# Performance work log

Hardware: AMD Instinct MI355X
Metric: run time of the kernel (lower is better)

## Reference

```python
import jax, jax.numpy as jnp
import numpy as np

NUM_HEADS = 12

def setup_inputs() -> dict:
    key = jax.random.key(0)
    k1, k2, k3, k4 = jax.random.split(key, 4)
    B, N, D = 8, 1024, 768
    x = jax.random.normal(k1, (B, N, D), dtype=jnp.float32)
    mask = jax.random.randint(k2, (B, N), 0, 2, dtype=jnp.int32)
    Wqkv = jax.random.normal(k3, (3 * D, D), dtype=jnp.float32) * (D ** -0.5)
    Wproj = jax.random.normal(k4, (D, D), dtype=jnp.float32) * (D ** -0.5)
    bproj = jnp.zeros((D,), dtype=jnp.float32)
    return {"x": x, "mask": mask, "Wqkv": Wqkv, "Wproj": Wproj, "bproj": bproj}

def reference(x, mask, Wqkv, Wproj, bproj):
    B, N, D = x.shape
    H = NUM_HEADS
    hd = D // H
    scale = hd ** -0.5
    # QKV projection (no bias), split into q,k,v of shape [B,H,N,hd]
    qkv = jnp.einsum('bnd,ed->bne', x, Wqkv).reshape(B, N, 3, H, hd)
    qkv = jnp.transpose(qkv, (2, 0, 3, 1, 4))
    q, k, v = qkv[0], qkv[1], qkv[2]
    # padding mask: attend where both query and key are valid; masked-out
    # (padded) query rows attend only to themselves (diagonal) to avoid NaNs
    m = mask.astype(bool)  # [B,N]
    pair = m[:, None, :, None] & m[:, None, None, :]          # [B,1,N,N]
    diag = jnp.eye(N, dtype=bool)[None, None]                 # [1,1,N,N]
    attn_mask = pair | (diag & ~m[:, None, :, None])          # [B,1,N,N]
    scores = jnp.einsum('bhnd,bhmd->bhnm', q, k) * scale      # [B,H,N,N]
    scores = jnp.where(attn_mask, scores, jnp.finfo(scores.dtype).min)
    attn = jax.nn.softmax(scores, axis=-1)
    out = jnp.einsum('bhnm,bhmd->bhnd', attn, v)
    out = jnp.transpose(out, (0, 2, 1, 3)).reshape(B, N, D)
    out = jnp.einsum('bnd,ed->bne', out, Wproj) + bproj
    return out
```

## Files before the change

kernel.cpp:

```cpp
#include <hip/hip_runtime.h>
#include <hip/hip_bf16.h>
#include <stdint.h>


typedef unsigned short u16;
typedef __attribute__((ext_vector_type(8))) short short8;
typedef __attribute__((ext_vector_type(4))) float f32x4;

#define MFMA16(a, b, c) __builtin_amdgcn_mfma_f32_16x16x32_bf16((a), (b), (c), 0, 0, 0)

static __device__ __forceinline__ float bf2f(u16 u) {
    return __uint_as_float(((unsigned int)u) << 16);
}
static __device__ __forceinline__ u16 f2bf(float f) {
    __hip_bfloat16 h = __float2bfloat16(f);
    return *(u16*)&h;
}
static __device__ __forceinline__ void gld16(const u16* g, u16* l) {
  __builtin_amdgcn_global_load_lds(
      (const __attribute__((address_space(1))) void*)g,
      (__attribute__((address_space(3))) void*)l, 16, 0, 0);
}

__global__ __launch_bounds__(256) void cvt_bf16(
    const float* __restrict__ s0, u16* __restrict__ d0, int n0,
    const float* __restrict__ s1, u16* __restrict__ d1, int n1,
    const float* __restrict__ s2, u16* __restrict__ d2, int n2) {
  int i = (blockIdx.x * 256 + threadIdx.x) * 4;
  const float* s; u16* d;
  if (i < n0) { s = s0 + i; d = d0 + i; }
  else if ((i -= n0) < n1) { s = s1 + i; d = d1 + i; }
  else if ((i -= n1) < n2) { s = s2 + i; d = d2 + i; }
  else return;
  float4 v = *(const float4*)s;
  ushort4 o;
  o.x = f2bf(v.x); o.y = f2bf(v.y); o.z = f2bf(v.z); o.w = f2bf(v.w);
  *(ushort4*)d = o;
}

template<int K, int LDC, bool BF16OUT>
__global__ __launch_bounds__(256) void gemm_bt(
    const u16* __restrict__ A,
    const u16* __restrict__ B,
    void* __restrict__ Cout,
    const float* __restrict__ bias) {
  __shared__ u16 As[128 * 32];
  __shared__ u16 Bs[128 * 32];
  const int tid = threadIdx.x;
  const int w = tid >> 6, l = tid & 63;
  const int lane16 = l & 15, quad = l >> 4;
  const int i0 = blockIdx.y * 128, j0 = blockIdx.x * 128;
  const int mh = (w & 1) * 64;
  const int nh = (w >> 1) * 64;

  f32x4 acc[4][4];
  #pragma unroll
  for (int mt = 0; mt < 4; mt++)
    #pragma unroll
    for (int nt = 0; nt < 4; nt++) acc[mt][nt] = (f32x4){0.f, 0.f, 0.f, 0.f};

  for (int kt = 0; kt < K / 32; kt++) {
    const int k0 = kt * 32;
    __syncthreads();
    #pragma unroll
    for (int s = 0; s < 2; s++) {
      int idx = tid + s * 256;
      int row = idx >> 2, c8 = (idx & 3) * 8;
      gld16(&A[(size_t)(i0 + row) * K + k0 + c8], &As[row * 32 + c8]);
      gld16(&B[(size_t)(j0 + row) * K + k0 + c8], &Bs[row * 32 + c8]);
    }
    __syncthreads();

    short8 af[4], bf[4];
    #pragma unroll
    for (int mt = 0; mt < 4; mt++)
      af[mt] = *(const short8*)&As[(mh + mt * 16 + lane16) * 32 + quad * 8];
    #pragma unroll
    for (int nt = 0; nt < 4; nt++)
      bf[nt] = *(const short8*)&Bs[(nh + nt * 16 + lane16) * 32 + quad * 8];
    #pragma unroll
    for (int mt = 0; mt < 4; mt++)
      #pragma unroll
      for (int nt = 0; nt < 4; nt++)
        acc[mt][nt] = MFMA16(af[mt], bf[nt], acc[mt][nt]);
  }

  #pragma unroll
  for (int mt = 0; mt < 4; mt++) {
    #pragma unroll
    for (int nt = 0; nt < 4; nt++) {
      int col = j0 + nh + nt * 16 + lane16;
      #pragma unroll
      for (int r = 0; r < 4; r++) {
        int row = i0 + mh + mt * 16 + quad * 4 + r;
        if (BF16OUT) {
          ((u16*)Cout)[(size_t)row * LDC + col] = f2bf(acc[mt][nt][r]);
        } else {
          ((float*)Cout)[(size_t)row * LDC + col] = acc[mt][nt][r] + bias[col];
        }
      }
    }
  }
}

__global__ __launch_bounds__(256, 3) void attn_mfma(
    const u16* __restrict__ qkv,
    const int* __restrict__ mask,
    u16* __restrict__ ctx) {
  __shared__ u16 Ks[64][72];
  __shared__ u16 Vt[64][72];
  __shared__ u16 Ps[4][32][72];
  __shared__ float mkb[64];
  __shared__ int mqs[128];

  const int tid = threadIdx.x;
  const int w = tid >> 6, l = tid & 63;
  const int lane16 = l & 15, quad = l >> 4;
  const int bh = blockIdx.x >> 3, rb = blockIdx.x & 7;
  const int b = bh / 12, h = bh % 12;
  const int n0 = rb * 128;
  const int baseRow = b * 1024;

  if (tid < 128) mqs[tid] = mask[baseRow + n0 + tid];

  short8 qfrag[2][2];
  #pragma unroll
  for (int mt = 0; mt < 2; mt++) {
    const u16* qp = qkv + (size_t)(baseRow + n0 + w*32 + mt*16 + lane16) * 2304 + h*64;
    #pragma unroll
    for (int ks = 0; ks < 2; ks++)
      qfrag[mt][ks] = *(const short8*)(qp + ks*32 + quad*8);
  }

  f32x4 oacc[2][4];
  #pragma unroll
  for (int mt = 0; mt < 2; mt++)
    #pragma unroll
    for (int nt = 0; nt < 4; nt++) oacc[mt][nt] = (f32x4){0.f, 0.f, 0.f, 0.f};
  float lsum[2][4];
  #pragma unroll
  for (int mt = 0; mt < 2; mt++)
    #pragma unroll
    for (int r = 0; r < 4; r++) lsum[mt][r] = 0.f;

  __syncthreads();
  int mqbits = 0;
  #pragma unroll
  for (int mt = 0; mt < 2; mt++)
    #pragma unroll
    for (int r = 0; r < 4; r++)
      mqbits |= (mqs[w*32 + mt*16 + quad*4 + r] ? 1 : 0) << (mt*4 + r);

  const float K1 = 0.18033688011112043f;
  const float K0 = -23.083120654223415f;

  for (int c = 0; c < 16; c++) {
    __syncthreads();
    {
      int key = tid >> 2, ds = (tid & 3) * 16;
      const u16* kp = qkv + (size_t)(baseRow + c*64 + key) * 2304 + 768 + h*64 + ds;
      *(uint4*)&Ks[key][ds]     = *(const uint4*)kp;
      *(uint4*)&Ks[key][ds + 8] = *(const uint4*)(kp + 8);
      int kA = (tid & 31) * 2, dg = tid >> 5;
      const u16* vp = qkv + (size_t)(baseRow + c*64 + kA) * 2304 + 1536 + h*64 + dg*8;
      uint4 r0 = *(const uint4*)vp;
      uint4 r1 = *(const uint4*)(vp + 2304);
      const u16* va = (const u16*)&r0;
      const u16* vb = (const u16*)&r1;
      #pragma unroll
      for (int j = 0; j < 8; j++)
        *(unsigned int*)&Vt[dg*8 + j][kA] = (unsigned int)va[j] | ((unsigned int)vb[j] << 16);
      if (tid < 64) mkb[tid] = mask[baseRow + c*64 + tid] ? 0.f : -1e38f;
    }
    __syncthreads();

    f32x4 sacc[2][4];
    #pragma unroll
    for (int mt = 0; mt < 2; mt++)
      #pragma unroll
      for (int t = 0; t < 4; t++) sacc[mt][t] = (f32x4){0.f, 0.f, 0.f, 0.f};
    #pragma unroll
    for (int ks = 0; ks < 2; ks++) {
      short8 kf[4];
      #pragma unroll
      for (int t = 0; t < 4; t++)
        kf[t] = *(const short8*)&Ks[t*16 + lane16][ks*32 + quad*8];
      #pragma unroll
      for (int mt = 0; mt < 2; mt++)
        #pragma unroll
        for (int t = 0; t < 4; t++)
          sacc[mt][t] = MFMA16(qfrag[mt][ks], kf[t], sacc[mt][t]);
    }

    #pragma unroll
    for (int t = 0; t < 4; t++) {
      float bias = mkb[t*16 + lane16];
      int cg = c*64 + t*16 + lane16;
      #pragma unroll
      for (int mt = 0; mt < 2; mt++) {
        #pragma unroll
        for (int r = 0; r < 4; r++) {
          float e = __builtin_amdgcn_exp2f(fmaf(sacc[mt][t][r], K1, K0) + bias);
          int rg = n0 + w*32 + mt*16 + quad*4 + r;
          if (!((mqbits >> (mt*4 + r)) & 1)) e = (cg == rg) ? 1.0f : 0.0f;
          lsum[mt][r] += e;
          Ps[w][mt*16 + quad*4 + r][t*16 + lane16] = f2bf(e);
        }
      }
    }

    #pragma unroll
    for (int kc = 0; kc < 2; kc++) {
      short8 pf[2], vf[4];
      #pragma unroll
      for (int mt = 0; mt < 2; mt++)
        pf[mt] = *(const short8*)&Ps[w][mt*16 + lane16][kc*32 + quad*8];
      #pragma unroll
      for (int nt = 0; nt < 4; nt++)
        vf[nt] = *(const short8*)&Vt[nt*16 + lane16][kc*32 + quad*8];
      #pragma unroll
      for (int mt = 0; mt < 2; mt++)
        #pragma unroll
        for (int nt = 0; nt < 4; nt++)
          oacc[mt][nt] = MFMA16(pf[mt], vf[nt], oacc[mt][nt]);
    }
  }

  float linv[2][4];
  #pragma unroll
  for (int mt = 0; mt < 2; mt++)
    #pragma unroll
    for (int r = 0; r < 4; r++) {
      float s = lsum[mt][r];
      s += __shfl_xor(s, 1); s += __shfl_xor(s, 2);
      s += __shfl_xor(s, 4); s += __shfl_xor(s, 8);
      linv[mt][r] = 1.0f / s;
    }
  #pragma unroll
  for (int mt = 0; mt < 2; mt++) {
    #pragma unroll
    for (int nt = 0; nt < 4; nt++) {
      #pragma unroll
      for (int r = 0; r < 4; r++) {
        int rg = n0 + w*32 + mt*16 + quad*4 + r;
        ctx[(size_t)(baseRow + rg) * 768 + h*64 + nt*16 + lane16] =
            f2bf(oacc[mt][nt][r] * linv[mt][r]);
      }
    }
  }
}

extern "C" void kernel_launch(void* const* d_in, const int* in_sizes, int n_in,
                              void* d_out, int out_size, void* d_ws, size_t ws_size,
                              hipStream_t stream) {
  const float* x     = (const float*)d_in[0];
  const int*   mask  = (const int*)d_in[1];
  const float* Wqkv  = (const float*)d_in[2];
  const float* Wproj = (const float*)d_in[3];
  const float* bproj = (const float*)d_in[4];
  float* out = (float*)d_out;

  const int NX = 8192 * 768;
  const int NQ = 2304 * 768;
  const int NP = 768 * 768;

  char* wsb = (char*)d_ws;
  u16* qkv    = (u16*)wsb;
  u16* ctx    = (u16*)(wsb + (size_t)8192 * 2304 * 2);
  u16* xb     = (u16*)(wsb + (size_t)8192 * 2304 * 2 + (size_t)8192 * 768 * 2);
  u16* wqkvb  = xb + NX;
  u16* wprojb = wqkvb + NQ;

  int cvt_blocks = ((NX + NQ + NP) / 4 + 255) / 256;
  cvt_bf16<<<dim3(cvt_blocks), 256, 0, stream>>>(x, xb, NX, Wqkv, wqkvb, NQ, Wproj, wprojb, NP);

  gemm_bt<768, 2304, true><<<dim3(18, 64), 256, 0, stream>>>(xb, wqkvb, qkv, nullptr);
  attn_mfma<<<dim3(768), 256, 0, stream>>>(qkv, mask, ctx);
  gemm_bt<768, 768, false><<<dim3(6, 64), 256, 0, stream>>>(ctx, wprojb, out, bproj);
}
```

Measured before the change: 207.5 us.

## Double-buffer K/V tiles with register prefetch and transpose score MFMA

The attention kernel now double-buffers K, V and the key-mask bias in shared memory and prefetches the tile two chunks ahead into registers. This overlaps global loads with compute and cuts the loop to one barrier per chunk. The score MFMA operands are swapped (K times Q), so each lane holds four consecutive keys for one query and can write P as packed 8-byte stores; the row sum is reduced across quads and redistributed by shuffle. LDS use roughly doubles and launch bounds drop from 3 to 2 blocks per CU, which can lower occupancy.

```diff
diff --git a/kernel.cpp b/kernel.cpp
--- a/kernel.cpp
+++ b/kernel.cpp
@@ -103,14 +103,14 @@
   }
 }
 
-__global__ __launch_bounds__(256, 3) void attn_mfma(
+__global__ __launch_bounds__(256, 2) void attn_mfma(
     const u16* __restrict__ qkv,
     const int* __restrict__ mask,
     u16* __restrict__ ctx) {
-  __shared__ u16 Ks[64][72];
-  __shared__ u16 Vt[64][72];
+  __shared__ u16 Ks[2][64][72];
+  __shared__ u16 Vt[2][64][72];
   __shared__ u16 Ps[4][32][72];
-  __shared__ float mkb[64];
+  __shared__ float mkb[2][64];
   __shared__ int mqs[128];
 
   const int tid = threadIdx.x;
@@ -121,91 +121,107 @@
   const int n0 = rb * 128;
   const int baseRow = b * 1024;
 
+  const int key_s = tid >> 2, ds_s = (tid & 3) * 16;
+  const int kA_s = (tid & 31) * 2, dg_s = tid >> 5;
+
   if (tid < 128) mqs[tid] = mask[baseRow + n0 + tid];
 
   short8 qfrag[2][2];
   #pragma unroll
-  for (int mt = 0; mt < 2; mt++) {
-    const u16* qp = qkv + (size_t)(baseRow + n0 + w*32 + mt*16 + lane16) * 2304 + h*64;
+  for (int qt = 0; qt < 2; qt++) {
+    const u16* qp = qkv + (size_t)(baseRow + n0 + w*32 + qt*16 + lane16) * 2304 + h*64;
     #pragma unroll
     for (int ks = 0; ks < 2; ks++)
-      qfrag[mt][ks] = *(const short8*)(qp + ks*32 + quad*8);
+      qfrag[qt][ks] = *(const short8*)(qp + ks*32 + quad*8);
   }
 
   f32x4 oacc[2][4];
   #pragma unroll
-  for (int mt = 0; mt < 2; mt++)
-    #pragma unroll
-    for (int nt = 0; nt < 4; nt++) oacc[mt][nt] = (f32x4){0.f, 0.f, 0.f, 0.f};
-  float lsum[2][4];
-  #pragma unroll
-  for (int mt = 0; mt < 2; mt++)
-    #pragma unroll
-    for (int r = 0; r < 4; r++) lsum[mt][r] = 0.f;
-
+  for (int qt = 0; qt < 2; qt++)
+    #pragma unroll
+    for (int nt = 0; nt < 4; nt++) oacc[qt][nt] = (f32x4){0.f, 0.f, 0.f, 0.f};
+  float lsum[2] = {0.f, 0.f};
+
+  uint4 kr0[2], kr1[2], vr0[2], vr1[2];
+  int mkv[2];
+
+  auto issue = [&](int c, int rbuf) {
+    const u16* kp = qkv + (size_t)(baseRow + c*64 + key_s) * 2304 + 768 + h*64 + ds_s;
+    kr0[rbuf] = *(const uint4*)kp;
+    kr1[rbuf] = *(const uint4*)(kp + 8);
+    const u16* vp = qkv + (size_t)(baseRow + c*64 + kA_s) * 2304 + 1536 + h*64 + dg_s*8;
+    vr0[rbuf] = *(const uint4*)vp;
+    vr1[rbuf] = *(const uint4*)(vp + 2304);
+    mkv[rbuf] = (tid < 64) ? mask[baseRow + c*64 + tid] : 0;
+  };
+  auto commit = [&](int c, int rbuf) {
+    int lb = c & 1;
+    *(uint4*)&Ks[lb][key_s][ds_s]     = kr0[rbuf];
+    *(uint4*)&Ks[lb][key_s][ds_s + 8] = kr1[rbuf];
+    const u16* va = (const u16*)&vr0[rbuf];
+    const u16* vb = (const u16*)&vr1[rbuf];
+    #pragma unroll
+    for (int j = 0; j < 8; j++)
+      *(unsigned int*)&Vt[lb][dg_s*8 + j][kA_s] =
+          (unsigned int)va[j] | ((unsigned int)vb[j] << 16);
+    if (tid < 64) mkb[lb][tid] = mkv[rbuf] ? 0.f : -1e38f;
+  };
+
+  issue(0, 0); commit(0, 0); issue(1, 1);
   __syncthreads();
-  int mqbits = 0;
-  #pragma unroll
-  for (int mt = 0; mt < 2; mt++)
-    #pragma unroll
-    for (int r = 0; r < 4; r++)
-      mqbits |= (mqs[w*32 + mt*16 + quad*4 + r] ? 1 : 0) << (mt*4 + r);
+
+  int qrg[2]; int mqv[2];
+  #pragma unroll
+  for (int qt = 0; qt < 2; qt++) {
+    qrg[qt] = n0 + w*32 + qt*16 + lane16;
+    mqv[qt] = mqs[w*32 + qt*16 + lane16];
+  }
 
   const float K1 = 0.18033688011112043f;
   const float K0 = -23.083120654223415f;
 
   for (int c = 0; c < 16; c++) {
     __syncthreads();
-    {
-      int key = tid >> 2, ds = (tid & 3) * 16;
-      const u16* kp = qkv + (size_t)(baseRow + c*64 + key) * 2304 + 768 + h*64 + ds;
-      *(uint4*)&Ks[key][ds]     = *(const uint4*)kp;
-      *(uint4*)&Ks[key][ds + 8] = *(const uint4*)(kp + 8);
-      int kA = (tid & 31) * 2, dg = tid >> 5;
-      const u16* vp = qkv + (size_t)(baseRow + c*64 + kA) * 2304 + 1536 + h*64 + dg*8;
-      uint4 r0 = *(const uint4*)vp;
-      uint4 r1 = *(const uint4*)(vp + 2304);
-      const u16* va = (const u16*)&r0;
-      const u16* vb = (const u16*)&r1;
-      #pragma unroll
-      for (int j = 0; j < 8; j++)
-        *(unsigned int*)&Vt[dg*8 + j][kA] = (unsigned int)va[j] | ((unsigned int)vb[j] << 16);
-      if (tid < 64) mkb[tid] = mask[baseRow + c*64 + tid] ? 0.f : -1e38f;
-    }
-    __syncthreads();
-
-    f32x4 sacc[2][4];
-    #pragma unroll
-    for (int mt = 0; mt < 2; mt++)
-      #pragma unroll
-      for (int t = 0; t < 4; t++) sacc[mt][t] = (f32x4){0.f, 0.f, 0.f, 0.f};
-    #pragma unroll
-    for (int ks = 0; ks < 2; ks++) {
-      short8 kf[4];
-      #pragma unroll
-      for (int t = 0; t < 4; t++)
-        kf[t] = *(const short8*)&Ks[t*16 + lane16][ks*32 + quad*8];
-      #pragma unroll
-      for (int mt = 0; mt < 2; mt++)
+    if (c < 15) commit(c + 1, (c + 1) & 1);
+    if (c < 14) issue(c + 2, c & 1);
+    const int lb = c & 1;
+
+    short8 kf[4][2];
+    #pragma unroll
+    for (int kt = 0; kt < 4; kt++)
+      #pragma unroll
+      for (int ks = 0; ks < 2; ks++)
+        kf[kt][ks] = *(const short8*)&Ks[lb][kt*16 + lane16][ks*32 + quad*8];
+    f32x4 sacc[4][2];
+    #pragma unroll
+    for (int kt = 0; kt < 4; kt++)
+      #pragma unroll
+      for (int qt = 0; qt < 2; qt++) sacc[kt][qt] = (f32x4){0.f, 0.f, 0.f, 0.f};
+    #pragma unroll
+    for (int ks = 0; ks < 2; ks++)
+      #pragma unroll
+      for (int kt = 0; kt < 4; kt++)
         #pragma unroll
-        for (int t = 0; t < 4; t++)
-          sacc[mt][t] = MFMA16(qfrag[mt][ks], kf[t], sacc[mt][t]);
-    }
-
-    #pragma unroll
-    for (int t = 0; t < 4; t++) {
-      float bias = mkb[t*16 + lane16];
-      int cg = c*64 + t*16 + lane16;
-      #pragma unroll
-      for (int mt = 0; mt < 2; mt++) {
+        for (int qt = 0; qt < 2; qt++)
+          sacc[kt][qt] = MFMA16(kf[kt][ks], qfrag[qt][ks], sacc[kt][qt]);
+
+    #pragma unroll
+    for (int kt = 0; kt < 4; kt++) {
+      #pragma unroll
+      for (int qt = 0; qt < 2; qt++) {
+        u16 pk[4];
         #pragma unroll
         for (int r = 0; r < 4; r++) {
-          float e = __builtin_amdgcn_exp2f(fmaf(sacc[mt][t][r], K1, K0) + bias);
-          int rg = n0 + w*32 + mt*16 + quad*4 + r;
-          if (!((mqbits >> (mt*4 + r)) & 1)) e = (cg == rg) ? 1.0f : 0.0f;
-          lsum[mt][r] += e;
-          Ps[w][mt*16 + quad*4 + r][t*16 + lane16] = f2bf(e);
+          int keyl = kt*16 + quad*4 + r;
+          float e = __builtin_amdgcn_exp2f(fmaf(sacc[kt][qt][r], K1, K0) + mkb[lb][keyl]);
+          if (!mqv[qt]) e = ((c*64 + keyl) == qrg[qt]) ? 1.0f : 0.0f;
+          lsum[qt] += e;
+          pk[r] = f2bf(e);
         }
+        unsigned int lo = (unsigned int)pk[0] | ((unsigned int)pk[1] << 16);
+        unsigned int hi = (unsigned int)pk[2] | ((unsigned int)pk[3] << 16);
+        uint2 pv; pv.x = lo; pv.y = hi;
+        *(uint2*)&Ps[w][qt*16 + lane16][kt*16 + quad*4] = pv;
       }
     }
 
@@ -213,38 +229,38 @@
     for (int kc = 0; kc < 2; kc++) {
       short8 pf[2], vf[4];
       #pragma unroll
-      for (int mt = 0; mt < 2; mt++)
-        pf[mt] = *(const short8*)&Ps[w][mt*16 + lane16][kc*32 + quad*8];
+      for (int qt = 0; qt < 2; qt++)
+        pf[qt] = *(const short8*)&Ps[w][qt*16 + lane16][kc*32 + quad*8];
       #pragma unroll
       for (int nt = 0; nt < 4; nt++)
-        vf[nt] = *(const short8*)&Vt[nt*16 + lane16][kc*32 + quad*8];
-      #pragma unroll
-      for (int mt = 0; mt < 2; mt++)
+        vf[nt] = *(const short8*)&Vt[lb][nt*16 + lane16][kc*32 + quad*8];
+      #pragma unroll
+      for (int qt = 0; qt < 2; qt++)
         #pragma unroll
         for (int nt = 0; nt < 4; nt++)
-          oacc[mt][nt] = MFMA16(pf[mt], vf[nt], oacc[mt][nt]);
+          oacc[qt][nt] = MFMA16(pf[qt], vf[nt], oacc[qt][nt]);
     }
   }
 
   float linv[2][4];
   #pragma unroll
-  for (int mt = 0; mt < 2; mt++)
-    #pragma unroll
-    for (int r = 0; r < 4; r++) {
-      float s = lsum[mt][r];
-      s += __shfl_xor(s, 1); s += __shfl_xor(s, 2);
-      s += __shfl_xor(s, 4); s += __shfl_xor(s, 8);
-      linv[mt][r] = 1.0f / s;
-    }
-  #pragma unroll
-  for (int mt = 0; mt < 2; mt++) {
+  for (int qt = 0; qt < 2; qt++) {
+    float s = lsum[qt];
+    s += __shfl_xor(s, 16);
+    s += __shfl_xor(s, 32);
+    #pragma unroll
+    for (int r = 0; r < 4; r++)
+      linv[qt][r] = 1.0f / __shfl(s, quad*4 + r);
+  }
+  #pragma unroll
+  for (int qt = 0; qt < 2; qt++) {
     #pragma unroll
     for (int nt = 0; nt < 4; nt++) {
       #pragma unroll
       for (int r = 0; r < 4; r++) {
-        int rg = n0 + w*32 + mt*16 + quad*4 + r;
+        int rg = n0 + w*32 + qt*16 + quad*4 + r;
         ctx[(size_t)(baseRow + rg) * 768 + h*64 + nt*16 + lane16] =
-            f2bf(oacc[mt][nt][r] * linv[mt][r]);
+            f2bf(oacc[qt][nt][r] * linv[qt][r]);
       }
     }
   }
```

Result: slower. 246.4 us (+18.7%).

## Prefetch next K/V tile into registers, hoist masked-row handling to epilogue

Applied to the files above, without the earlier changes.

The attention kernel now issues global loads for the next K/V tile into registers before the current tile's MFMA work and writes them to LDS afterward, so load latency overlaps with compute. Masked query rows no longer get a per-element diagonal select inside the softmax loop. Their output is instead copied directly from the V row in the epilogue, which matches the reference because such a row attends only to itself. The block index mapping is changed so rb varies slowest, and launch bounds are raised to 4 waves per SIMD. The prefetch keeps extra values live in registers, which could conflict with the higher occupancy target.

```diff
diff --git a/kernel.cpp b/kernel.cpp
--- a/kernel.cpp
+++ b/kernel.cpp
@@ -103,7 +103,7 @@
   }
 }
 
-__global__ __launch_bounds__(256, 3) void attn_mfma(
+__global__ __launch_bounds__(256, 4) void attn_mfma(
     const u16* __restrict__ qkv,
     const int* __restrict__ mask,
     u16* __restrict__ ctx) {
@@ -116,11 +116,16 @@
   const int tid = threadIdx.x;
   const int w = tid >> 6, l = tid & 63;
   const int lane16 = l & 15, quad = l >> 4;
-  const int bh = blockIdx.x >> 3, rb = blockIdx.x & 7;
+  const int idx = blockIdx.x;
+  const int bh = idx % 96;
+  const int rb = idx / 96;
   const int b = bh / 12, h = bh % 12;
   const int n0 = rb * 128;
   const int baseRow = b * 1024;
 
+  const int key_s = tid >> 2, ds_s = (tid & 3) * 16;
+  const int kA_s = (tid & 31) * 2, dg_s = tid >> 5;
+
   if (tid < 128) mqs[tid] = mask[baseRow + n0 + tid];
 
   short8 qfrag[2][2];
@@ -143,36 +148,38 @@
     #pragma unroll
     for (int r = 0; r < 4; r++) lsum[mt][r] = 0.f;
 
+  uint4 kr0, kr1, vr0, vr1;
+  int mkv;
+  auto issue = [&](int c) {
+    const u16* kp = qkv + (size_t)(baseRow + c*64 + key_s) * 2304 + 768 + h*64 + ds_s;
+    kr0 = *(const uint4*)kp;
+    kr1 = *(const uint4*)(kp + 8);
+    const u16* vp = qkv + (size_t)(baseRow + c*64 + kA_s) * 2304 + 1536 + h*64 + dg_s*8;
+    vr0 = *(const uint4*)vp;
+    vr1 = *(const uint4*)(vp + 2304);
+    mkv = (tid < 64) ? mask[baseRow + c*64 + tid] : 0;
+  };
+  auto commit = [&]() {
+    *(uint4*)&Ks[key_s][ds_s]     = kr0;
+    *(uint4*)&Ks[key_s][ds_s + 8] = kr1;
+    const u16* va = (const u16*)&vr0;
+    const u16* vb = (const u16*)&vr1;
+    #pragma unroll
+    for (int j = 0; j < 8; j++)
+      *(unsigned int*)&Vt[dg_s*8 + j][kA_s] =
+          (unsigned int)va[j] | ((unsigned int)vb[j] << 16);
+    if (tid < 64) mkb[tid] = mkv ? 0.f : -1e38f;
+  };
+
+  issue(0);
+  commit();
   __syncthreads();
-  int mqbits = 0;
-  #pragma unroll
-  for (int mt = 0; mt < 2; mt++)
-    #pragma unroll
-    for (int r = 0; r < 4; r++)
-      mqbits |= (mqs[w*32 + mt*16 + quad*4 + r] ? 1 : 0) << (mt*4 + r);
 
   const float K1 = 0.18033688011112043f;
   const float K0 = -23.083120654223415f;
 
   for (int c = 0; c < 16; c++) {
-    __syncthreads();
-    {
-      int key = tid >> 2, ds = (tid & 3) * 16;
-      const u16* kp = qkv + (size_t)(baseRow + c*64 + key) * 2304 + 768 + h*64 + ds;
-      *(uint4*)&Ks[key][ds]     = *(const uint4*)kp;
-      *(uint4*)&Ks[key][ds + 8] = *(const uint4*)(kp + 8);
-      int kA = (tid & 31) * 2, dg = tid >> 5;
-      const u16* vp = qkv + (size_t)(baseRow + c*64 + kA) * 2304 + 1536 + h*64 + dg*8;
-      uint4 r0 = *(const uint4*)vp;
-      uint4 r1 = *(const uint4*)(vp + 2304);
-      const u16* va = (const u16*)&r0;
-      const u16* vb = (const u16*)&r1;
-      #pragma unroll
-      for (int j = 0; j < 8; j++)
-        *(unsigned int*)&Vt[dg*8 + j][kA] = (unsigned int)va[j] | ((unsigned int)vb[j] << 16);
-      if (tid < 64) mkb[tid] = mask[baseRow + c*64 + tid] ? 0.f : -1e38f;
-    }
-    __syncthreads();
+    if (c < 15) issue(c + 1);
 
     f32x4 sacc[2][4];
     #pragma unroll
@@ -195,14 +202,11 @@
     #pragma unroll
     for (int t = 0; t < 4; t++) {
       float bias = mkb[t*16 + lane16];
-      int cg = c*64 + t*16 + lane16;
       #pragma unroll
       for (int mt = 0; mt < 2; mt++) {
         #pragma unroll
         for (int r = 0; r < 4; r++) {
           float e = __builtin_amdgcn_exp2f(fmaf(sacc[mt][t][r], K1, K0) + bias);
-          int rg = n0 + w*32 + mt*16 + quad*4 + r;
-          if (!((mqbits >> (mt*4 + r)) & 1)) e = (cg == rg) ? 1.0f : 0.0f;
           lsum[mt][r] += e;
           Ps[w][mt*16 + quad*4 + r][t*16 + lane16] = f2bf(e);
         }
@@ -223,6 +227,12 @@
         #pragma unroll
         for (int nt = 0; nt < 4; nt++)
           oacc[mt][nt] = MFMA16(pf[mt], vf[nt], oacc[mt][nt]);
+    }
+
+    __syncthreads();
+    if (c < 15) {
+      commit();
+      __syncthreads();
     }
   }
 
@@ -239,12 +249,19 @@
   #pragma unroll
   for (int mt = 0; mt < 2; mt++) {
     #pragma unroll
-    for (int nt = 0; nt < 4; nt++) {
-      #pragma unroll
-      for (int r = 0; r < 4; r++) {
-        int rg = n0 + w*32 + mt*16 + quad*4 + r;
-        ctx[(size_t)(baseRow + rg) * 768 + h*64 + nt*16 + lane16] =
-            f2bf(oacc[mt][nt][r] * linv[mt][r]);
+    for (int r = 0; r < 4; r++) {
+      int rl = w*32 + mt*16 + quad*4 + r;
+      int rg = n0 + rl;
+      int mq = mqs[rl];
+      #pragma unroll
+      for (int nt = 0; nt < 4; nt++) {
+        u16 outv;
+        if (mq) {
+          outv = f2bf(oacc[mt][nt][r] * linv[mt][r]);
+        } else {
+          outv = qkv[(size_t)(baseRow + rg) * 2304 + 1536 + h*64 + nt*16 + lane16];
+        }
+        ctx[(size_t)(baseRow + rg) * 768 + h*64 + nt*16 + lane16] = outv;
       }
     }
   }
```

Result: slower. 236.2 us (+13.8%).
